# Optimization experiments

Hardware: AMD Instinct MI355X
Metric: run time of the kernel (lower is better)

## Reference

```python
import jax, jax.numpy as jnp
import numpy as np


def setup_inputs() -> dict:
    key = jax.random.key(0)
    ks = jax.random.split(key, 4)
    B, S, H = 1, 2048, 2048
    E, I = 32, 768
    scale_h = 1.0 / np.sqrt(H)
    scale_i = 1.0 / np.sqrt(I)
    return {
        "hidden_states": jax.random.normal(ks[0], (B, S, H), dtype=jnp.float32),
        "gate_w": jax.random.normal(ks[1], (E, H), dtype=jnp.float32) * scale_h,
        "gate_up_proj": jax.random.normal(ks[2], (E, H, 2 * I), dtype=jnp.float32) * scale_h,
        "down_proj": jax.random.normal(ks[3], (E, I, H), dtype=jnp.float32) * scale_i,
    }


TOP_K = 4


def reference(hidden_states, gate_w, gate_up_proj, down_proj):
    B, S, H = hidden_states.shape
    x = hidden_states.reshape(-1, H)                      # [T, H]
    T = x.shape[0]

    # Router: softmax -> top-k -> renormalize -> scatter back to dense [T, E]
    router_logits = x @ gate_w.T                          # [T, E]
    probs = jax.nn.softmax(router_logits.astype(jnp.float32), axis=-1)
    top_w, top_idx = jax.lax.top_k(probs, TOP_K)          # [T, K]
    top_w = top_w / jnp.sum(top_w, axis=-1, keepdims=True)
    top_w = top_w.astype(x.dtype)
    router_weights = jnp.zeros_like(router_logits).at[
        jnp.arange(T)[:, None], top_idx
    ].set(top_w)                                          # [T, E]

    # Experts (eval path): every expert processes every token, then weight & sum.
    gate_up = jnp.einsum("th,ehi->eti", x, gate_up_proj)  # [E, T, 2I]
    gate, up = jnp.split(gate_up, 2, axis=-1)
    h = up * jax.nn.silu(gate)                            # [E, T, I]
    expert_out = jnp.einsum("eti,eih->eth", h, down_proj)  # [E, T, H]
    out = jnp.einsum("eth,te->th", expert_out, router_weights)  # [T, H]

    return out.reshape(B, S, H), router_logits
```

## Files before the change

kernel.cpp:

```cpp
#include <hip/hip_runtime.h>
#include <hip/hip_bf16.h>

#define T_TOK 2048
#define H_DIM 2048
#define E_NUM 32
#define I_DIM 768
#define TOPK  4
#define S4    (T_TOK * TOPK)

typedef __attribute__((ext_vector_type(8))) short bf16x8;
typedef __attribute__((ext_vector_type(4))) float f32x4;

__device__ __forceinline__ unsigned pk2(float a, float b) {
    __hip_bfloat16 ha = __float2bfloat16(a);
    __hip_bfloat16 hb = __float2bfloat16(b);
    unsigned short ua = *(unsigned short*)&ha;
    unsigned short ub = *(unsigned short*)&hb;
    return (unsigned)ua | ((unsigned)ub << 16);
}

__device__ __forceinline__ void gld16(const void* g, void* l) {
    __builtin_amdgcn_global_load_lds(
        (const __attribute__((address_space(1))) void*)g,
        (__attribute__((address_space(3))) void*)l, 16, 0, 0);
}

__global__ __launch_bounds__(256) void zero_kernel(uint4* __restrict__ p, int n16)
{
    int i = blockIdx.x * 256 + threadIdx.x;
    if (i < n16) p[i] = (uint4){0u, 0u, 0u, 0u};
}

__global__ __launch_bounds__(64) void router_kernel(
    const float* __restrict__ x, const float* __restrict__ gate_w,
    float* __restrict__ logits_out, int* __restrict__ cnt,
    int* __restrict__ tok_list, float* __restrict__ tok_w)
{
    const int t = blockIdx.x;
    const int lane = threadIdx.x;
    __shared__ float xs[H_DIM];
    const float4* __restrict__ xv = (const float4*)(x + (size_t)t * H_DIM);
    float4* xsv = (float4*)xs;
#pragma unroll
    for (int i = 0; i < H_DIM / 4 / 64; ++i) xsv[lane + i * 64] = xv[lane + i * 64];
    __syncthreads();

    const int e = lane & 31;
    const int half = lane >> 5;
    const float4* __restrict__ wv = (const float4*)(gate_w + (size_t)e * H_DIM) + half * (H_DIM / 8);
    const float4* __restrict__ xh = ((const float4*)xs) + half * (H_DIM / 8);
    float acc = 0.f;
#pragma unroll 4
    for (int i = 0; i < H_DIM / 8; ++i) {
        float4 w4 = wv[i], x4 = xh[i];
        acc += w4.x * x4.x + w4.y * x4.y + w4.z * x4.z + w4.w * x4.w;
    }
    acc += __shfl_xor(acc, 32, 64);
    if (lane < 32) logits_out[(size_t)t * E_NUM + e] = acc;

    float v = acc;
    float topv[TOPK]; int topi[TOPK];
#pragma unroll
    for (int r = 0; r < TOPK; ++r) {
        float bv = v; int bi = e;
#pragma unroll
        for (int off = 16; off >= 1; off >>= 1) {
            float ov = __shfl_xor(bv, off, 32);
            int   oi = __shfl_xor(bi, off, 32);
            if (ov > bv || (ov == bv && oi < bi)) { bv = ov; bi = oi; }
        }
        topv[r] = bv; topi[r] = bi;
        if (e == bi) v = -1e30f;
    }
    if (lane == 0) {
        float w[TOPK]; float s = 0.f;
#pragma unroll
        for (int r = 0; r < TOPK; ++r) { w[r] = expf(topv[r] - topv[0]); s += w[r]; }
        float inv = 1.f / s;
#pragma unroll
        for (int r = 0; r < TOPK; ++r) {
            int pos = atomicAdd(&cnt[topi[r]], 1);
            tok_list[topi[r] * T_TOK + pos] = t;
            tok_w  [topi[r] * T_TOK + pos] = w[r] * inv;
        }
    }
}

__global__ void scan_kernel(const int* __restrict__ cnt, int* __restrict__ slot_base)
{
    if (threadIdx.x == 0) {
        int s = 0;
        for (int e = 0; e < E_NUM; ++e) { slot_base[e] = s; s += cnt[e]; }
        slot_base[E_NUM] = s;
    }
}

__global__ __launch_bounds__(256) void gather_kernel(
    const float* __restrict__ x, const int* __restrict__ cnt,
    const int* __restrict__ slot_base, const int* __restrict__ tok_list,
    unsigned short* __restrict__ xg_t)
{
    const int e = blockIdx.x;
    const int count = cnt[e];
    const int m0 = blockIdx.y * 8;
    if (m0 >= count) return;
    const int s8   = threadIdx.x >> 5;
    const int kc31 = threadIdx.x & 31;
    const int m = m0 + s8;
    if (m >= count) return;
    const int tok  = tok_list[e * T_TOK + m];
    const int slot = slot_base[e] + m;
    const float* __restrict__ src = x + (size_t)tok * H_DIM;
#pragma unroll
    for (int kcq = 0; kcq < 8; ++kcq) {
        const int kc = kcq * 32 + kc31;
        float4 a = *(const float4*)(src + kc * 8);
        float4 b = *(const float4*)(src + kc * 8 + 4);
        uint4 o;
        o.x = pk2(a.x, a.y); o.y = pk2(a.z, a.w);
        o.z = pk2(b.x, b.y); o.w = pk2(b.z, b.w);
        *(uint4*)(xg_t + ((size_t)kc * S4 + slot) * 8) = o;
    }
}

#define GU_NT (H_DIM / 32)
__global__ __launch_bounds__(512, 6) void gateup_mfma(
    const unsigned short* __restrict__ xg_t, const float* __restrict__ gup_w,
    const int* __restrict__ cnt, const int* __restrict__ slot_base,
    const float* __restrict__ tok_w, unsigned short* __restrict__ h_t)
{
    const int e  = blockIdx.x;
    const int nt = blockIdx.y;
    const int mt = blockIdx.z;
    const int count = cnt[e];
    if (mt * 256 >= count) return;
    const int tid  = threadIdx.x;
    const int lane = tid & 63;
    const int w    = tid >> 6;
    const int base = slot_base[e];
    const int l16  = lane & 15, lg = lane >> 4;

    __shared__ unsigned short As[2][4 * 256 * 8];
    __shared__ unsigned short Bg[2][4 * 32 * 8];
    __shared__ unsigned short Bu[2][4 * 32 * 8];
    __shared__ float wls[256];

    if (tid < 256) {
        int m = mt * 256 + tid; if (m >= count) m = count - 1;
        wls[tid] = tok_w[e * T_TOK + m];
    }

    const int kc = w >> 1;
    const int q0 = (w & 1) * 2;
    int r0 = mt * 256 + q0 * 64 + lane;       if (r0 >= count) r0 = count - 1;
    int r1 = mt * 256 + (q0 + 1) * 64 + lane; if (r1 >= count) r1 = count - 1;
    const unsigned short* ag0 = xg_t + (size_t)kc * (S4 * 8) + (size_t)(base + r0) * 8;
    const unsigned short* ag1 = xg_t + (size_t)kc * (S4 * 8) + (size_t)(base + r1) * 8;
    const int al0 = (kc * 256 + q0 * 64) * 8;
    const int al1 = (kc * 256 + (q0 + 1) * 64) * 8;
    const size_t astep = (size_t)4 * S4 * 8;

    const bool bstage = tid < 256;
    const int bhalf = (tid >> 7) & 1;
    const int t7    = tid & 127;
    const int kb    = (t7 >> 3) * 2;
    const int n4    = (t7 & 7) * 4;
    const int kcb   = kb >> 3;
    const int k8    = kb & 7;
    const float* __restrict__ bsrc =
        gup_w + ((size_t)e * H_DIM + kb) * (2 * I_DIM) + (size_t)bhalf * I_DIM + nt * 32 + n4;

    const int aoff = (lg * 256 + w * 32 + l16) * 8;
    const int boff = (lg * 32 + l16) * 8;

    f32x4 accg[2][2], accu[2][2];
#pragma unroll
    for (int i = 0; i < 2; ++i)
#pragma unroll
        for (int f = 0; f < 2; ++f) { accg[i][f] = {0.f,0.f,0.f,0.f}; accu[i][f] = {0.f,0.f,0.f,0.f}; }

    float4 pr0, pr1;

    gld16(ag0, &As[0][al0]);
    gld16(ag1, &As[0][al1]);
    if (bstage) {
        pr0 = *(const float4*)bsrc;
        pr1 = *(const float4*)(bsrc + 2 * I_DIM);
        unsigned short* bw = bhalf ? &Bu[0][0] : &Bg[0][0];
        float p0[4] = {pr0.x, pr0.y, pr0.z, pr0.w};
        float p1[4] = {pr1.x, pr1.y, pr1.z, pr1.w};
#pragma unroll
        for (int j = 0; j < 4; ++j)
            *(unsigned*)&bw[((kcb * 32 + n4 + j) * 8) + k8] = pk2(p0[j], p1[j]);
    }

    for (int ks = 0; ks < GU_NT; ++ks) {
        const int cur = ks & 1;
        __syncthreads();
        if (ks + 1 < GU_NT) {
            gld16(ag0 + (size_t)(ks + 1) * astep, &As[cur ^ 1][al0]);
            gld16(ag1 + (size_t)(ks + 1) * astep, &As[cur ^ 1][al1]);
            if (bstage) {
                const float* bs_ = bsrc + (size_t)(ks + 1) * 32 * (2 * I_DIM);
                pr0 = *(const float4*)bs_;
                pr1 = *(const float4*)(bs_ + 2 * I_DIM);
            }
        }
        {
            const unsigned short* af_ = &As[cur][aoff];
            const unsigned short* bg_ = &Bg[cur][boff];
            const unsigned short* bu_ = &Bu[cur][boff];
            bf16x8 vg0 = *(const bf16x8*)(bg_);
            bf16x8 vg1 = *(const bf16x8*)(bg_ + 128);
            bf16x8 vu0 = *(const bf16x8*)(bu_);
            bf16x8 vu1 = *(const bf16x8*)(bu_ + 128);
#pragma unroll
            for (int i = 0; i < 2; ++i) {
                bf16x8 va = *(const bf16x8*)(af_ + i * 16 * 8);
                accg[i][0] = __builtin_amdgcn_mfma_f32_16x16x32_bf16(va, vg0, accg[i][0], 0, 0, 0);
                accg[i][1] = __builtin_amdgcn_mfma_f32_16x16x32_bf16(va, vg1, accg[i][1], 0, 0, 0);
                accu[i][0] = __builtin_amdgcn_mfma_f32_16x16x32_bf16(va, vu0, accu[i][0], 0, 0, 0);
                accu[i][1] = __builtin_amdgcn_mfma_f32_16x16x32_bf16(va, vu1, accu[i][1], 0, 0, 0);
            }
        }
        if (ks + 1 < GU_NT && bstage) {
            unsigned short* bw = bhalf ? &Bu[cur ^ 1][0] : &Bg[cur ^ 1][0];
            float p0[4] = {pr0.x, pr0.y, pr0.z, pr0.w};
            float p1[4] = {pr1.x, pr1.y, pr1.z, pr1.w};
#pragma unroll
            for (int j = 0; j < 4; ++j)
                *(unsigned*)&bw[((kcb * 32 + n4 + j) * 8) + k8] = pk2(p0[j], p1[j]);
        }
    }

#pragma unroll
    for (int i = 0; i < 2; ++i) {
        const int mloc = w * 32 + i * 16 + lg * 4;
#pragma unroll
        for (int r = 0; r < 4; ++r) {
            const int mrow = mt * 256 + mloc + r;
            if (mrow < count) {
                const float wgt = wls[mloc + r];
                const size_t slot = (size_t)(base + mrow);
#pragma unroll
                for (int f = 0; f < 2; ++f) {
                    const int col = nt * 32 + f * 16 + l16;
                    float g = accg[i][f][r], u = accu[i][f][r];
                    float sv = g / (1.f + expf(-g));
                    __hip_bfloat16 hb = __float2bfloat16(wgt * u * sv);
                    h_t[((size_t)(col >> 3) * S4 + slot) * 8 + (col & 7)] = *(unsigned short*)&hb;
                }
            }
        }
    }
}

#define DN_NT (I_DIM / 32)
__global__ __launch_bounds__(512, 6) void down_mfma(
    const unsigned short* __restrict__ h_t, const float* __restrict__ down_w,
    const int* __restrict__ cnt, const int* __restrict__ slot_base,
    const int* __restrict__ tok_list, float* __restrict__ out)
{
    const int e  = blockIdx.x;
    const int nt = blockIdx.y;
    const int mt = blockIdx.z;
    const int count = cnt[e];
    if (mt * 256 >= count) return;
    const int tid  = threadIdx.x;
    const int lane = tid & 63;
    const int w    = tid >> 6;
    const int base = slot_base[e];
    const int l16  = lane & 15, lg = lane >> 4;

    __shared__ unsigned short As[2][4 * 256 * 8];
    __shared__ unsigned short Bs[2][4 * 64 * 8];
    __shared__ int toks[256];

    if (tid < 256) {
        int m = mt * 256 + tid; if (m >= count) m = count - 1;
        toks[tid] = tok_list[e * T_TOK + m];
    }

    const int kc = w >> 1;
    const int q0 = (w & 1) * 2;
    int r0 = mt * 256 + q0 * 64 + lane;       if (r0 >= count) r0 = count - 1;
    int r1 = mt * 256 + (q0 + 1) * 64 + lane; if (r1 >= count) r1 = count - 1;
    const unsigned short* ag0 = h_t + (size_t)kc * (S4 * 8) + (size_t)(base + r0) * 8;
    const unsigned short* ag1 = h_t + (size_t)kc * (S4 * 8) + (size_t)(base + r1) * 8;
    const int al0 = (kc * 256 + q0 * 64) * 8;
    const int al1 = (kc * 256 + (q0 + 1) * 64) * 8;
    const size_t astep = (size_t)4 * S4 * 8;

    const bool bstage = tid < 256;
    const int t8  = tid & 255;
    const int kb  = (t8 >> 4) * 2;
    const int n4  = (t8 & 15) * 4;
    const int kcb = kb >> 3;
    const int k8  = kb & 7;
    const float* __restrict__ bsrc =
        down_w + ((size_t)e * I_DIM + kb) * H_DIM + nt * 64 + n4;

    const int aoff = (lg * 256 + w * 32 + l16) * 8;
    const int boff = (lg * 64 + l16) * 8;

    f32x4 acc[2][4];
#pragma unroll
    for (int i = 0; i < 2; ++i)
#pragma unroll
        for (int f = 0; f < 4; ++f) acc[i][f] = {0.f,0.f,0.f,0.f};

    float4 pr0, pr1;

    gld16(ag0, &As[0][al0]);
    gld16(ag1, &As[0][al1]);
    if (bstage) {
        pr0 = *(const float4*)bsrc;
        pr1 = *(const float4*)(bsrc + H_DIM);
        float p0[4] = {pr0.x, pr0.y, pr0.z, pr0.w};
        float p1[4] = {pr1.x, pr1.y, pr1.z, pr1.w};
#pragma unroll
        for (int j = 0; j < 4; ++j)
            *(unsigned*)&Bs[0][((kcb * 64 + n4 + j) * 8) + k8] = pk2(p0[j], p1[j]);
    }

    for (int ks = 0; ks < DN_NT; ++ks) {
        const int cur = ks & 1;
        __syncthreads();
        if (ks + 1 < DN_NT) {
            gld16(ag0 + (size_t)(ks + 1) * astep, &As[cur ^ 1][al0]);
            gld16(ag1 + (size_t)(ks + 1) * astep, &As[cur ^ 1][al1]);
            if (bstage) {
                const float* bs_ = bsrc + (size_t)(ks + 1) * 32 * H_DIM;
                pr0 = *(const float4*)bs_;
                pr1 = *(const float4*)(bs_ + H_DIM);
            }
        }
        {
            const unsigned short* af_ = &As[cur][aoff];
            const unsigned short* bf_ = &Bs[cur][boff];
            bf16x8 vb0 = *(const bf16x8*)(bf_);
            bf16x8 vb1 = *(const bf16x8*)(bf_ + 128);
            bf16x8 vb2 = *(const bf16x8*)(bf_ + 256);
            bf16x8 vb3 = *(const bf16x8*)(bf_ + 384);
#pragma unroll
            for (int i = 0; i < 2; ++i) {
                bf16x8 va = *(const bf16x8*)(af_ + i * 16 * 8);
                acc[i][0] = __builtin_amdgcn_mfma_f32_16x16x32_bf16(va, vb0, acc[i][0], 0, 0, 0);
                acc[i][1] = __builtin_amdgcn_mfma_f32_16x16x32_bf16(va, vb1, acc[i][1], 0, 0, 0);
                acc[i][2] = __builtin_amdgcn_mfma_f32_16x16x32_bf16(va, vb2, acc[i][2], 0, 0, 0);
                acc[i][3] = __builtin_amdgcn_mfma_f32_16x16x32_bf16(va, vb3, acc[i][3], 0, 0, 0);
            }
        }
        if (ks + 1 < DN_NT && bstage) {
            float p0[4] = {pr0.x, pr0.y, pr0.z, pr0.w};
            float p1[4] = {pr1.x, pr1.y, pr1.z, pr1.w};
#pragma unroll
            for (int j = 0; j < 4; ++j)
                *(unsigned*)&Bs[cur ^ 1][((kcb * 64 + n4 + j) * 8) + k8] = pk2(p0[j], p1[j]);
        }
    }

#pragma unroll
    for (int i = 0; i < 2; ++i) {
        const int mloc = w * 32 + i * 16 + lg * 4;
#pragma unroll
        for (int r = 0; r < 4; ++r) {
            const int mrow = mt * 256 + mloc + r;
            if (mrow < count) {
                const int tok = toks[mloc + r];
#pragma unroll
                for (int f = 0; f < 4; ++f) {
                    const int col = nt * 64 + f * 16 + l16;
                    atomicAdd(&out[(size_t)tok * H_DIM + col], acc[i][f][r]);
                }
            }
        }
    }
}

extern "C" void kernel_launch(void* const* d_in, const int* in_sizes, int n_in,
                              void* d_out, int out_size, void* d_ws, size_t ws_size,
                              hipStream_t stream) {
    const float* x      = (const float*)d_in[0];
    const float* gate_w = (const float*)d_in[1];
    const float* gup_w  = (const float*)d_in[2];
    const float* down_w = (const float*)d_in[3];
    float* out    = (float*)d_out;

    char* wsp = (char*)d_ws;
    int*   cnt       = (int*)(wsp);
    int*   slot_base = (int*)(wsp + 256);
    int*   tok_list  = (int*)(wsp + 4096);
    float* tok_w     = (float*)(wsp + 4096 + (size_t)E_NUM * T_TOK * 4);
    unsigned short* xg_t = (unsigned short*)(wsp + (1u << 20));
    unsigned short* h_t  = (unsigned short*)(wsp + (1u << 20) + (size_t)S4 * H_DIM * 2);

    const int n16 = T_TOK * H_DIM / 4;
    zero_kernel<<<(n16 + 255) / 256, 256, 0, stream>>>((uint4*)out, n16);
    hipMemsetAsync(cnt, 0, 256, stream);

    router_kernel<<<T_TOK, 64, 0, stream>>>(x, gate_w, out + (size_t)T_TOK * H_DIM,
                                            cnt, tok_list, tok_w);
    scan_kernel<<<1, 64, 0, stream>>>(cnt, slot_base);
    gather_kernel<<<dim3(E_NUM, 256), 256, 0, stream>>>(x, cnt, slot_base, tok_list, xg_t);
    gateup_mfma<<<dim3(E_NUM, 24, 8), 512, 0, stream>>>(
        xg_t, gup_w, cnt, slot_base, tok_w, h_t);
    down_mfma<<<dim3(E_NUM, 32, 8), 512, 0, stream>>>(
        h_t, down_w, cnt, slot_base, tok_list, out);
}
```

Measured before the change: 518.0 us.

## Loop over token tiles inside each expert block with smaller 128-row tiles

```diff
diff --git a/kernel.cpp b/kernel.cpp
--- a/kernel.cpp
+++ b/kernel.cpp
@@ -124,44 +124,32 @@
 }
 
 #define GU_NT (H_DIM / 32)
-__global__ __launch_bounds__(512, 6) void gateup_mfma(
+__global__ __launch_bounds__(256, 6) void gateup_mfma(
     const unsigned short* __restrict__ xg_t, const float* __restrict__ gup_w,
     const int* __restrict__ cnt, const int* __restrict__ slot_base,
     const float* __restrict__ tok_w, unsigned short* __restrict__ h_t)
 {
     const int e  = blockIdx.x;
     const int nt = blockIdx.y;
-    const int mt = blockIdx.z;
     const int count = cnt[e];
-    if (mt * 256 >= count) return;
+    const int nmt = (count + 127) >> 7;
     const int tid  = threadIdx.x;
     const int lane = tid & 63;
     const int w    = tid >> 6;
     const int base = slot_base[e];
     const int l16  = lane & 15, lg = lane >> 4;
 
-    __shared__ unsigned short As[2][4 * 256 * 8];
+    __shared__ unsigned short As[2][4 * 128 * 8];
     __shared__ unsigned short Bg[2][4 * 32 * 8];
     __shared__ unsigned short Bu[2][4 * 32 * 8];
-    __shared__ float wls[256];
-
-    if (tid < 256) {
-        int m = mt * 256 + tid; if (m >= count) m = count - 1;
-        wls[tid] = tok_w[e * T_TOK + m];
-    }
-
-    const int kc = w >> 1;
-    const int q0 = (w & 1) * 2;
-    int r0 = mt * 256 + q0 * 64 + lane;       if (r0 >= count) r0 = count - 1;
-    int r1 = mt * 256 + (q0 + 1) * 64 + lane; if (r1 >= count) r1 = count - 1;
-    const unsigned short* ag0 = xg_t + (size_t)kc * (S4 * 8) + (size_t)(base + r0) * 8;
-    const unsigned short* ag1 = xg_t + (size_t)kc * (S4 * 8) + (size_t)(base + r1) * 8;
-    const int al0 = (kc * 256 + q0 * 64) * 8;
-    const int al1 = (kc * 256 + (q0 + 1) * 64) * 8;
+    __shared__ float wls[128];
+
+    const unsigned short* agb = xg_t + (size_t)w * (S4 * 8) + (size_t)base * 8;
+    const int al0 = (w * 128 + 0) * 8;
+    const int al1 = (w * 128 + 64) * 8;
     const size_t astep = (size_t)4 * S4 * 8;
 
-    const bool bstage = tid < 256;
-    const int bhalf = (tid >> 7) & 1;
+    const int bhalf = tid >> 7;
     const int t7    = tid & 127;
     const int kb    = (t7 >> 3) * 2;
     const int n4    = (t7 & 7) * 4;
@@ -170,208 +158,215 @@
     const float* __restrict__ bsrc =
         gup_w + ((size_t)e * H_DIM + kb) * (2 * I_DIM) + (size_t)bhalf * I_DIM + nt * 32 + n4;
 
-    const int aoff = (lg * 256 + w * 32 + l16) * 8;
+    const int aoff = (lg * 128 + w * 32 + l16) * 8;
     const int boff = (lg * 32 + l16) * 8;
 
-    f32x4 accg[2][2], accu[2][2];
-#pragma unroll
-    for (int i = 0; i < 2; ++i)
-#pragma unroll
-        for (int f = 0; f < 2; ++f) { accg[i][f] = {0.f,0.f,0.f,0.f}; accu[i][f] = {0.f,0.f,0.f,0.f}; }
-
-    float4 pr0, pr1;
-
-    gld16(ag0, &As[0][al0]);
-    gld16(ag1, &As[0][al1]);
-    if (bstage) {
-        pr0 = *(const float4*)bsrc;
-        pr1 = *(const float4*)(bsrc + 2 * I_DIM);
-        unsigned short* bw = bhalf ? &Bu[0][0] : &Bg[0][0];
-        float p0[4] = {pr0.x, pr0.y, pr0.z, pr0.w};
-        float p1[4] = {pr1.x, pr1.y, pr1.z, pr1.w};
-#pragma unroll
-        for (int j = 0; j < 4; ++j)
-            *(unsigned*)&bw[((kcb * 32 + n4 + j) * 8) + k8] = pk2(p0[j], p1[j]);
-    }
-
-    for (int ks = 0; ks < GU_NT; ++ks) {
-        const int cur = ks & 1;
+    for (int mt = 0; mt < nmt; ++mt) {
         __syncthreads();
-        if (ks + 1 < GU_NT) {
-            gld16(ag0 + (size_t)(ks + 1) * astep, &As[cur ^ 1][al0]);
-            gld16(ag1 + (size_t)(ks + 1) * astep, &As[cur ^ 1][al1]);
-            if (bstage) {
+        if (tid < 128) {
+            int m = mt * 128 + tid; if (m >= count) m = count - 1;
+            wls[tid] = tok_w[e * T_TOK + m];
+        }
+        int r0 = mt * 128 + lane;      if (r0 >= count) r0 = count - 1;
+        int r1 = mt * 128 + 64 + lane; if (r1 >= count) r1 = count - 1;
+        const unsigned short* ag0 = agb + (size_t)r0 * 8;
+        const unsigned short* ag1 = agb + (size_t)r1 * 8;
+
+        f32x4 accg[2][2], accu[2][2];
+#pragma unroll
+        for (int i = 0; i < 2; ++i)
+#pragma unroll
+            for (int f = 0; f < 2; ++f) { accg[i][f] = {0.f,0.f,0.f,0.f}; accu[i][f] = {0.f,0.f,0.f,0.f}; }
+
+        float4 pr0, pr1;
+
+        gld16(ag0, &As[0][al0]);
+        gld16(ag1, &As[0][al1]);
+        {
+            pr0 = *(const float4*)bsrc;
+            pr1 = *(const float4*)(bsrc + 2 * I_DIM);
+            unsigned short* bw = bhalf ? &Bu[0][0] : &Bg[0][0];
+            float p0[4] = {pr0.x, pr0.y, pr0.z, pr0.w};
+            float p1[4] = {pr1.x, pr1.y, pr1.z, pr1.w};
+#pragma unroll
+            for (int j = 0; j < 4; ++j)
+                *(unsigned*)&bw[((kcb * 32 + n4 + j) * 8) + k8] = pk2(p0[j], p1[j]);
+        }
+
+        for (int ks = 0; ks < GU_NT; ++ks) {
+            const int cur = ks & 1;
+            __syncthreads();
+            if (ks + 1 < GU_NT) {
+                gld16(ag0 + (size_t)(ks + 1) * astep, &As[cur ^ 1][al0]);
+                gld16(ag1 + (size_t)(ks + 1) * astep, &As[cur ^ 1][al1]);
                 const float* bs_ = bsrc + (size_t)(ks + 1) * 32 * (2 * I_DIM);
                 pr0 = *(const float4*)bs_;
                 pr1 = *(const float4*)(bs_ + 2 * I_DIM);
             }
-        }
-        {
-            const unsigned short* af_ = &As[cur][aoff];
-            const unsigned short* bg_ = &Bg[cur][boff];
-            const unsigned short* bu_ = &Bu[cur][boff];
-            bf16x8 vg0 = *(const bf16x8*)(bg_);
-            bf16x8 vg1 = *(const bf16x8*)(bg_ + 128);
-            bf16x8 vu0 = *(const bf16x8*)(bu_);
-            bf16x8 vu1 = *(const bf16x8*)(bu_ + 128);
-#pragma unroll
-            for (int i = 0; i < 2; ++i) {
-                bf16x8 va = *(const bf16x8*)(af_ + i * 16 * 8);
-                accg[i][0] = __builtin_amdgcn_mfma_f32_16x16x32_bf16(va, vg0, accg[i][0], 0, 0, 0);
-                accg[i][1] = __builtin_amdgcn_mfma_f32_16x16x32_bf16(va, vg1, accg[i][1], 0, 0, 0);
-                accu[i][0] = __builtin_amdgcn_mfma_f32_16x16x32_bf16(va, vu0, accu[i][0], 0, 0, 0);
-                accu[i][1] = __builtin_amdgcn_mfma_f32_16x16x32_bf16(va, vu1, accu[i][1], 0, 0, 0);
-            }
-        }
-        if (ks + 1 < GU_NT && bstage) {
-            unsigned short* bw = bhalf ? &Bu[cur ^ 1][0] : &Bg[cur ^ 1][0];
-            float p0[4] = {pr0.x, pr0.y, pr0.z, pr0.w};
-            float p1[4] = {pr1.x, pr1.y, pr1.z, pr1.w};
-#pragma unroll
-            for (int j = 0; j < 4; ++j)
-                *(unsigned*)&bw[((kcb * 32 + n4 + j) * 8) + k8] = pk2(p0[j], p1[j]);
-        }
-    }
-
-#pragma unroll
-    for (int i = 0; i < 2; ++i) {
-        const int mloc = w * 32 + i * 16 + lg * 4;
-#pragma unroll
-        for (int r = 0; r < 4; ++r) {
-            const int mrow = mt * 256 + mloc + r;
-            if (mrow < count) {
-                const float wgt = wls[mloc + r];
-                const size_t slot = (size_t)(base + mrow);
-#pragma unroll
-                for (int f = 0; f < 2; ++f) {
-                    const int col = nt * 32 + f * 16 + l16;
-                    float g = accg[i][f][r], u = accu[i][f][r];
-                    float sv = g / (1.f + expf(-g));
-                    __hip_bfloat16 hb = __float2bfloat16(wgt * u * sv);
-                    h_t[((size_t)(col >> 3) * S4 + slot) * 8 + (col & 7)] = *(unsigned short*)&hb;
+            {
+                const unsigned short* af_ = &As[cur][aoff];
+                const unsigned short* bg_ = &Bg[cur][boff];
+                const unsigned short* bu_ = &Bu[cur][boff];
+                bf16x8 vg0 = *(const bf16x8*)(bg_);
+                bf16x8 vg1 = *(const bf16x8*)(bg_ + 128);
+                bf16x8 vu0 = *(const bf16x8*)(bu_);
+                bf16x8 vu1 = *(const bf16x8*)(bu_ + 128);
+#pragma unroll
+                for (int i = 0; i < 2; ++i) {
+                    bf16x8 va = *(const bf16x8*)(af_ + i * 16 * 8);
+                    accg[i][0] = __builtin_amdgcn_mfma_f32_16x16x32_bf16(va, vg0, accg[i][0], 0, 0, 0);
+                    accg[i][1] = __builtin_amdgcn_mfma_f32_16x16x32_bf16(va, vg1, accg[i][1], 0, 0, 0);
+                    accu[i][0] = __builtin_amdgcn_mfma_f32_16x16x32_bf16(va, vu0, accu[i][0], 0, 0, 0);
+                    accu[i][1] = __builtin_amdgcn_mfma_f32_16x16x32_bf16(va, vu1, accu[i][1], 0, 0, 0);
                 }
             }
+            if (ks + 1 < GU_NT) {
+                unsigned short* bw = bhalf ? &Bu[cur ^ 1][0] : &Bg[cur ^ 1][0];
+                float p0[4] = {pr0.x, pr0.y, pr0.z, pr0.w};
+                float p1[4] = {pr1.x, pr1.y, pr1.z, pr1.w};
+#pragma unroll
+                for (int j = 0; j < 4; ++j)
+                    *(unsigned*)&bw[((kcb * 32 + n4 + j) * 8) + k8] = pk2(p0[j], p1[j]);
+            }
+        }
+
+#pragma unroll
+        for (int i = 0; i < 2; ++i) {
+            const int mloc = w * 32 + i * 16 + lg * 4;
+#pragma unroll
+            for (int r = 0; r < 4; ++r) {
+                const int mrow = mt * 128 + mloc + r;
+                if (mrow < count) {
+                    const float wgt = wls[mloc + r];
+                    const size_t slot = (size_t)(base + mrow);
+#pragma unroll
+                    for (int f = 0; f < 2; ++f) {
+                        const int col = nt * 32 + f * 16 + l16;
+                        float g = accg[i][f][r], u = accu[i][f][r];
+                        float sv = g / (1.f + expf(-g));
+                        __hip_bfloat16 hb = __float2bfloat16(wgt * u * sv);
+                        h_t[((size_t)(col >> 3) * S4 + slot) * 8 + (col & 7)] = *(unsigned short*)&hb;
+                    }
+                }
+            }
         }
     }
 }
 
 #define DN_NT (I_DIM / 32)
-__global__ __launch_bounds__(512, 6) void down_mfma(
+__global__ __launch_bounds__(256, 6) void down_mfma(
     const unsigned short* __restrict__ h_t, const float* __restrict__ down_w,
     const int* __restrict__ cnt, const int* __restrict__ slot_base,
     const int* __restrict__ tok_list, float* __restrict__ out)
 {
     const int e  = blockIdx.x;
     const int nt = blockIdx.y;
-    const int mt = blockIdx.z;
     const int count = cnt[e];
-    if (mt * 256 >= count) return;
+    const int nmt = (count + 127) >> 7;
     const int tid  = threadIdx.x;
     const int lane = tid & 63;
     const int w    = tid >> 6;
     const int base = slot_base[e];
     const int l16  = lane & 15, lg = lane >> 4;
 
-    __shared__ unsigned short As[2][4 * 256 * 8];
+    __shared__ unsigned short As[2][4 * 128 * 8];
     __shared__ unsigned short Bs[2][4 * 64 * 8];
-    __shared__ int toks[256];
-
-    if (tid < 256) {
-        int m = mt * 256 + tid; if (m >= count) m = count - 1;
-        toks[tid] = tok_list[e * T_TOK + m];
-    }
-
-    const int kc = w >> 1;
-    const int q0 = (w & 1) * 2;
-    int r0 = mt * 256 + q0 * 64 + lane;       if (r0 >= count) r0 = count - 1;
-    int r1 = mt * 256 + (q0 + 1) * 64 + lane; if (r1 >= count) r1 = count - 1;
-    const unsigned short* ag0 = h_t + (size_t)kc * (S4 * 8) + (size_t)(base + r0) * 8;
-    const unsigned short* ag1 = h_t + (size_t)kc * (S4 * 8) + (size_t)(base + r1) * 8;
-    const int al0 = (kc * 256 + q0 * 64) * 8;
-    const int al1 = (kc * 256 + (q0 + 1) * 64) * 8;
+    __shared__ int toks[128];
+
+    const unsigned short* agb = h_t + (size_t)w * (S4 * 8) + (size_t)base * 8;
+    const int al0 = (w * 128 + 0) * 8;
+    const int al1 = (w * 128 + 64) * 8;
     const size_t astep = (size_t)4 * S4 * 8;
 
-    const bool bstage = tid < 256;
-    const int t8  = tid & 255;
-    const int kb  = (t8 >> 4) * 2;
-    const int n4  = (t8 & 15) * 4;
+    const int kb  = (tid >> 4) * 2;
+    const int n4  = (tid & 15) * 4;
     const int kcb = kb >> 3;
     const int k8  = kb & 7;
     const float* __restrict__ bsrc =
         down_w + ((size_t)e * I_DIM + kb) * H_DIM + nt * 64 + n4;
 
-    const int aoff = (lg * 256 + w * 32 + l16) * 8;
+    const int aoff = (lg * 128 + w * 32 + l16) * 8;
     const int boff = (lg * 64 + l16) * 8;
 
-    f32x4 acc[2][4];
-#pragma unroll
-    for (int i = 0; i < 2; ++i)
-#pragma unroll
-        for (int f = 0; f < 4; ++f) acc[i][f] = {0.f,0.f,0.f,0.f};
-
-    float4 pr0, pr1;
-
-    gld16(ag0, &As[0][al0]);
-    gld16(ag1, &As[0][al1]);
-    if (bstage) {
-        pr0 = *(const float4*)bsrc;
-        pr1 = *(const float4*)(bsrc + H_DIM);
-        float p0[4] = {pr0.x, pr0.y, pr0.z, pr0.w};
-        float p1[4] = {pr1.x, pr1.y, pr1.z, pr1.w};
-#pragma unroll
-        for (int j = 0; j < 4; ++j)
-            *(unsigned*)&Bs[0][((kcb * 64 + n4 + j) * 8) + k8] = pk2(p0[j], p1[j]);
-    }
-
-    for (int ks = 0; ks < DN_NT; ++ks) {
-        const int cur = ks & 1;
+    for (int mt = 0; mt < nmt; ++mt) {
         __syncthreads();
-        if (ks + 1 < DN_NT) {
-            gld16(ag0 + (size_t)(ks + 1) * astep, &As[cur ^ 1][al0]);
-            gld16(ag1 + (size_t)(ks + 1) * astep, &As[cur ^ 1][al1]);
-            if (bstage) {
+        if (tid < 128) {
+            int m = mt * 128 + tid; if (m >= count) m = count - 1;
+            toks[tid] = tok_list[e * T_TOK + m];
+        }
+        int r0 = mt * 128 + lane;      if (r0 >= count) r0 = count - 1;
+        int r1 = mt * 128 + 64 + lane; if (r1 >= count) r1 = count - 1;
+        const unsigned short* ag0 = agb + (size_t)r0 * 8;
+        const unsigned short* ag1 = agb + (size_t)r1 * 8;
+
+        f32x4 acc[2][4];
+#pragma unroll
+        for (int i = 0; i < 2; ++i)
+#pragma unroll
+            for (int f = 0; f < 4; ++f) acc[i][f] = {0.f,0.f,0.f,0.f};
+
+        float4 pr0, pr1;
+
+        gld16(ag0, &As[0][al0]);
+        gld16(ag1, &As[0][al1]);
+        {
+            pr0 = *(const float4*)bsrc;
+            pr1 = *(const float4*)(bsrc + H_DIM);
+            float p0[4] = {pr0.x, pr0.y, pr0.z, pr0.w};
+            float p1[4] = {pr1.x, pr1.y, pr1.z, pr1.w};
+#pragma unroll
+            for (int j = 0; j < 4; ++j)
+                *(unsigned*)&Bs[0][((kcb * 64 + n4 + j) * 8) + k8] = pk2(p0[j], p1[j]);
+        }
+
+        for (int ks = 0; ks < DN_NT; ++ks) {
+            const int cur = ks & 1;
+            __syncthreads();
+            if (ks + 1 < DN_NT) {
+                gld16(ag0 + (size_t)(ks + 1) * astep, &As[cur ^ 1][al0]);
+                gld16(ag1 + (size_t)(ks + 1) * astep, &As[cur ^ 1][al1]);
                 const float* bs_ = bsrc + (size_t)(ks + 1) * 32 * H_DIM;
                 pr0 = *(const float4*)bs_;
                 pr1 = *(const float4*)(bs_ + H_DIM);
             }
-        }
-        {
-            const unsigned short* af_ = &As[cur][aoff];
-            const unsigned short* bf_ = &Bs[cur][boff];
-            bf16x8 vb0 = *(const bf16x8*)(bf_);
-            bf16x8 vb1 = *(const bf16x8*)(bf_ + 128);
-            bf16x8 vb2 = *(const bf16x8*)(bf_ + 256);
-            bf16x8 vb3 = *(const bf16x8*)(bf_ + 384);
-#pragma unroll
-            for (int i = 0; i < 2; ++i) {
-                bf16x8 va = *(const bf16x8*)(af_ + i * 16 * 8);
-                acc[i][0] = __builtin_amdgcn_mfma_f32_16x16x32_bf16(va, vb0, acc[i][0], 0, 0, 0);
-                acc[i][1] = __builtin_amdgcn_mfma_f32_16x16x32_bf16(va, vb1, acc[i][1], 0, 0, 0);
-                acc[i][2] = __builtin_amdgcn_mfma_f32_16x16x32_bf16(va, vb2, acc[i][2], 0, 0, 0);
-                acc[i][3] = __builtin_amdgcn_mfma_f32_16x16x32_bf16(va, vb3, acc[i][3], 0, 0, 0);
-            }
-        }
-        if (ks + 1 < DN_NT && bstage) {
-            float p0[4] = {pr0.x, pr0.y, pr0.z, pr0.w};
-            float p1[4] = {pr1.x, pr1.y, pr1.z, pr1.w};
-#pragma unroll
-            for (int j = 0; j < 4; ++j)
-                *(unsigned*)&Bs[cur ^ 1][((kcb * 64 + n4 + j) * 8) + k8] = pk2(p0[j], p1[j]);
-        }
-    }
-
-#pragma unroll
-    for (int i = 0; i < 2; ++i) {
-        const int mloc = w * 32 + i * 16 + lg * 4;
-#pragma unroll
-        for (int r = 0; r < 4; ++r) {
-            const int mrow = mt * 256 + mloc + r;
-            if (mrow < count) {
-                const int tok = toks[mloc + r];
-#pragma unroll
-                for (int f = 0; f < 4; ++f) {
-                    const int col = nt * 64 + f * 16 + l16;
-                    atomicAdd(&out[(size_t)tok * H_DIM + col], acc[i][f][r]);
+            {
+                const unsigned short* af_ = &As[cur][aoff];
+                const unsigned short* bf_ = &Bs[cur][boff];
+                bf16x8 vb0 = *(const bf16x8*)(bf_);
+                bf16x8 vb1 = *(const bf16x8*)(bf_ + 128);
+                bf16x8 vb2 = *(const bf16x8*)(bf_ + 256);
+                bf16x8 vb3 = *(const bf16x8*)(bf_ + 384);
+#pragma unroll
+                for (int i = 0; i < 2; ++i) {
+                    bf16x8 va = *(const bf16x8*)(af_ + i * 16 * 8);
+                    acc[i][0] = __builtin_amdgcn_mfma_f32_16x16x32_bf16(va, vb0, acc[i][0], 0, 0, 0);
+                    acc[i][1] = __builtin_amdgcn_mfma_f32_16x16x32_bf16(va, vb1, acc[i][1], 0, 0, 0);
+                    acc[i][2] = __builtin_amdgcn_mfma_f32_16x16x32_bf16(va, vb2, acc[i][2], 0, 0, 0);
+                    acc[i][3] = __builtin_amdgcn_mfma_f32_16x16x32_bf16(va, vb3, acc[i][3], 0, 0, 0);
+                }
+            }
+            if (ks + 1 < DN_NT) {
+                float p0[4] = {pr0.x, pr0.y, pr0.z, pr0.w};
+                float p1[4] = {pr1.x, pr1.y, pr1.z, pr1.w};
+#pragma unroll
+                for (int j = 0; j < 4; ++j)
+                    *(unsigned*)&Bs[cur ^ 1][((kcb * 64 + n4 + j) * 8) + k8] = pk2(p0[j], p1[j]);
+            }
+        }
+
+#pragma unroll
+        for (int i = 0; i < 2; ++i) {
+            const int mloc = w * 32 + i * 16 + lg * 4;
+#pragma unroll
+            for (int r = 0; r < 4; ++r) {
+                const int mrow = mt * 128 + mloc + r;
+                if (mrow < count) {
+                    const int tok = toks[mloc + r];
+#pragma unroll
+                    for (int f = 0; f < 4; ++f) {
+                        const int col = nt * 64 + f * 16 + l16;
+                        atomicAdd(&out[(size_t)tok * H_DIM + col], acc[i][f][r]);
+                    }
                 }
             }
         }
@@ -403,8 +398,8 @@
                                             cnt, tok_list, tok_w);
     scan_kernel<<<1, 64, 0, stream>>>(cnt, slot_base);
     gather_kernel<<<dim3(E_NUM, 256), 256, 0, stream>>>(x, cnt, slot_base, tok_list, xg_t);
-    gateup_mfma<<<dim3(E_NUM, 24, 8), 512, 0, stream>>>(
+    gateup_mfma<<<dim3(E_NUM, 24), 256, 0, stream>>>(
         xg_t, gup_w, cnt, slot_base, tok_w, h_t);
-    down_mfma<<<dim3(E_NUM, 32, 8), 512, 0, stream>>>(
+    down_mfma<<<dim3(E_NUM, 32), 256, 0, stream>>>(
         h_t, down_w, cnt, slot_base, tok_list, out);
 }
```

Result: slower. 680.6 us (+31.4%).

## Flatten expert grids with XCD-aware expert swizzle and raise occupancy hints

Applied to the files above, without the earlier changes.

```diff
diff --git a/kernel.cpp b/kernel.cpp
--- a/kernel.cpp
+++ b/kernel.cpp
@@ -23,6 +23,10 @@
     __builtin_amdgcn_global_load_lds(
         (const __attribute__((address_space(1))) void*)g,
         (__attribute__((address_space(3))) void*)l, 16, 0, 0);
+}
+
+__device__ __forceinline__ int eswz(int bid) {
+    return (bid & 7) | (((bid >> 3) & 3) << 3);
 }
 
 __global__ __launch_bounds__(256) void zero_kernel(uint4* __restrict__ p, int n16)
@@ -100,9 +104,10 @@
     const int* __restrict__ slot_base, const int* __restrict__ tok_list,
     unsigned short* __restrict__ xg_t)
 {
-    const int e = blockIdx.x;
+    const int bid = blockIdx.x;
+    const int e = eswz(bid);
     const int count = cnt[e];
-    const int m0 = blockIdx.y * 8;
+    const int m0 = (bid >> 5) * 8;
     if (m0 >= count) return;
     const int s8   = threadIdx.x >> 5;
     const int kc31 = threadIdx.x & 31;
@@ -124,14 +129,16 @@
 }
 
 #define GU_NT (H_DIM / 32)
-__global__ __launch_bounds__(512, 6) void gateup_mfma(
+__global__ __launch_bounds__(512, 8) void gateup_mfma(
     const unsigned short* __restrict__ xg_t, const float* __restrict__ gup_w,
     const int* __restrict__ cnt, const int* __restrict__ slot_base,
     const float* __restrict__ tok_w, unsigned short* __restrict__ h_t)
 {
-    const int e  = blockIdx.x;
-    const int nt = blockIdx.y;
-    const int mt = blockIdx.z;
+    const int bid = blockIdx.x;
+    const int e    = eswz(bid);
+    const int rest = bid >> 5;
+    const int nt   = rest % 24;
+    const int mt   = rest / 24;
     const int count = cnt[e];
     if (mt * 256 >= count) return;
     const int tid  = threadIdx.x;
@@ -143,12 +150,6 @@
     __shared__ unsigned short As[2][4 * 256 * 8];
     __shared__ unsigned short Bg[2][4 * 32 * 8];
     __shared__ unsigned short Bu[2][4 * 32 * 8];
-    __shared__ float wls[256];
-
-    if (tid < 256) {
-        int m = mt * 256 + tid; if (m >= count) m = count - 1;
-        wls[tid] = tok_w[e * T_TOK + m];
-    }
 
     const int kc = w >> 1;
     const int q0 = (w & 1) * 2;
@@ -240,7 +241,7 @@
         for (int r = 0; r < 4; ++r) {
             const int mrow = mt * 256 + mloc + r;
             if (mrow < count) {
-                const float wgt = wls[mloc + r];
+                const float wgt = tok_w[e * T_TOK + mrow];
                 const size_t slot = (size_t)(base + mrow);
 #pragma unroll
                 for (int f = 0; f < 2; ++f) {
@@ -256,14 +257,16 @@
 }
 
 #define DN_NT (I_DIM / 32)
-__global__ __launch_bounds__(512, 6) void down_mfma(
+__global__ __launch_bounds__(512, 8) void down_mfma(
     const unsigned short* __restrict__ h_t, const float* __restrict__ down_w,
     const int* __restrict__ cnt, const int* __restrict__ slot_base,
     const int* __restrict__ tok_list, float* __restrict__ out)
 {
-    const int e  = blockIdx.x;
-    const int nt = blockIdx.y;
-    const int mt = blockIdx.z;
+    const int bid = blockIdx.x;
+    const int e    = eswz(bid);
+    const int rest = bid >> 5;
+    const int nt   = rest & 31;
+    const int mt   = rest >> 5;
     const int count = cnt[e];
     if (mt * 256 >= count) return;
     const int tid  = threadIdx.x;
@@ -274,12 +277,6 @@
 
     __shared__ unsigned short As[2][4 * 256 * 8];
     __shared__ unsigned short Bs[2][4 * 64 * 8];
-    __shared__ int toks[256];
-
-    if (tid < 256) {
-        int m = mt * 256 + tid; if (m >= count) m = count - 1;
-        toks[tid] = tok_list[e * T_TOK + m];
-    }
 
     const int kc = w >> 1;
     const int q0 = (w & 1) * 2;
@@ -367,7 +364,7 @@
         for (int r = 0; r < 4; ++r) {
             const int mrow = mt * 256 + mloc + r;
             if (mrow < count) {
-                const int tok = toks[mloc + r];
+                const int tok = tok_list[e * T_TOK + mrow];
 #pragma unroll
                 for (int f = 0; f < 4; ++f) {
                     const int col = nt * 64 + f * 16 + l16;
@@ -402,9 +399,9 @@
     router_kernel<<<T_TOK, 64, 0, stream>>>(x, gate_w, out + (size_t)T_TOK * H_DIM,
                                             cnt, tok_list, tok_w);
     scan_kernel<<<1, 64, 0, stream>>>(cnt, slot_base);
-    gather_kernel<<<dim3(E_NUM, 256), 256, 0, stream>>>(x, cnt, slot_base, tok_list, xg_t);
-    gateup_mfma<<<dim3(E_NUM, 24, 8), 512, 0, stream>>>(
+    gather_kernel<<<E_NUM * 256, 256, 0, stream>>>(x, cnt, slot_base, tok_list, xg_t);
+    gateup_mfma<<<E_NUM * 24 * 8, 512, 0, stream>>>(
         xg_t, gup_w, cnt, slot_base, tok_w, h_t);
-    down_mfma<<<dim3(E_NUM, 32, 8), 512, 0, stream>>>(
+    down_mfma<<<E_NUM * 32 * 8, 512, 0, stream>>>(
         h_t, down_w, cnt, slot_base, tok_list, out);
 }
```

Result: slower. 812.2 us (+56.8%).

## Load A fragments directly from global and stage B in 128-deep chunks

Applied to the files above, without the earlier changes.

```diff
diff --git a/kernel.cpp b/kernel.cpp
--- a/kernel.cpp
+++ b/kernel.cpp
@@ -19,11 +19,7 @@
     return (unsigned)ua | ((unsigned)ub << 16);
 }
 
-__device__ __forceinline__ void gld16(const void* g, void* l) {
-    __builtin_amdgcn_global_load_lds(
-        (const __attribute__((address_space(1))) void*)g,
-        (__attribute__((address_space(3))) void*)l, 16, 0, 0);
-}
+#define MFMA16(a, b, c) __builtin_amdgcn_mfma_f32_16x16x32_bf16(a, b, c, 0, 0, 0)
 
 __global__ __launch_bounds__(256) void zero_kernel(uint4* __restrict__ p, int n16)
 {
@@ -123,8 +119,8 @@
     }
 }
 
-#define GU_NT (H_DIM / 32)
-__global__ __launch_bounds__(512, 6) void gateup_mfma(
+#define GU_NC (H_DIM / 128)
+__global__ __launch_bounds__(512, 4) void gateup_mfma(
     const unsigned short* __restrict__ xg_t, const float* __restrict__ gup_w,
     const int* __restrict__ cnt, const int* __restrict__ slot_base,
     const float* __restrict__ tok_w, unsigned short* __restrict__ h_t)
@@ -140,9 +136,7 @@
     const int base = slot_base[e];
     const int l16  = lane & 15, lg = lane >> 4;
 
-    __shared__ unsigned short As[2][4 * 256 * 8];
-    __shared__ unsigned short Bg[2][4 * 32 * 8];
-    __shared__ unsigned short Bu[2][4 * 32 * 8];
+    __shared__ unsigned short Bls[2][2][16 * 32 * 8];
     __shared__ float wls[256];
 
     if (tid < 256) {
@@ -150,28 +144,35 @@
         wls[tid] = tok_w[e * T_TOK + m];
     }
 
-    const int kc = w >> 1;
-    const int q0 = (w & 1) * 2;
-    int r0 = mt * 256 + q0 * 64 + lane;       if (r0 >= count) r0 = count - 1;
-    int r1 = mt * 256 + (q0 + 1) * 64 + lane; if (r1 >= count) r1 = count - 1;
-    const unsigned short* ag0 = xg_t + (size_t)kc * (S4 * 8) + (size_t)(base + r0) * 8;
-    const unsigned short* ag1 = xg_t + (size_t)kc * (S4 * 8) + (size_t)(base + r1) * 8;
-    const int al0 = (kc * 256 + q0 * 64) * 8;
-    const int al1 = (kc * 256 + (q0 + 1) * 64) * 8;
-    const size_t astep = (size_t)4 * S4 * 8;
-
-    const bool bstage = tid < 256;
-    const int bhalf = (tid >> 7) & 1;
+    int m0 = mt * 256 + w * 32 + l16;      if (m0 >= count) m0 = count - 1;
+    int m1 = mt * 256 + w * 32 + 16 + l16; if (m1 >= count) m1 = count - 1;
+    const unsigned short* a0b = xg_t + (size_t)(base + m0) * 8;
+    const unsigned short* a1b = xg_t + (size_t)(base + m1) * 8;
+
+    const int bhalf = tid >> 8;
+    const int sub   = (tid >> 7) & 1;
     const int t7    = tid & 127;
     const int kb    = (t7 >> 3) * 2;
     const int n4    = (t7 & 7) * 4;
-    const int kcb   = kb >> 3;
     const int k8    = kb & 7;
-    const float* __restrict__ bsrc =
+    const int kbh   = kb >> 3;
+    const float* __restrict__ bbase =
         gup_w + ((size_t)e * H_DIM + kb) * (2 * I_DIM) + (size_t)bhalf * I_DIM + nt * 32 + n4;
 
-    const int aoff = (lg * 256 + w * 32 + l16) * 8;
-    const int boff = (lg * 32 + l16) * 8;
+    float4 sv0[2], sv1[2];
+
+#define GU_LOAD(C) do { _Pragma("unroll") for (int q2 = 0; q2 < 2; ++q2) { \
+        const int q = sub + q2 * 2; \
+        const float* s_ = bbase + (size_t)((C) * 128 + q * 32) * (2 * I_DIM); \
+        sv0[q2] = *(const float4*)s_; \
+        sv1[q2] = *(const float4*)(s_ + 2 * I_DIM); } } while (0)
+#define GU_WRITE(BUF) do { _Pragma("unroll") for (int q2 = 0; q2 < 2; ++q2) { \
+        const int q = sub + q2 * 2; \
+        unsigned short* bw_ = &Bls[BUF][bhalf][((q * 4 + kbh) * 32) * 8]; \
+        float p0[4] = {sv0[q2].x, sv0[q2].y, sv0[q2].z, sv0[q2].w}; \
+        float p1[4] = {sv1[q2].x, sv1[q2].y, sv1[q2].z, sv1[q2].w}; \
+        _Pragma("unroll") for (int j = 0; j < 4; ++j) \
+            *(unsigned*)&bw_[(n4 + j) * 8 + k8] = pk2(p0[j], p1[j]); } } while (0)
 
     f32x4 accg[2][2], accu[2][2];
 #pragma unroll
@@ -179,59 +180,37 @@
 #pragma unroll
         for (int f = 0; f < 2; ++f) { accg[i][f] = {0.f,0.f,0.f,0.f}; accu[i][f] = {0.f,0.f,0.f,0.f}; }
 
-    float4 pr0, pr1;
-
-    gld16(ag0, &As[0][al0]);
-    gld16(ag1, &As[0][al1]);
-    if (bstage) {
-        pr0 = *(const float4*)bsrc;
-        pr1 = *(const float4*)(bsrc + 2 * I_DIM);
-        unsigned short* bw = bhalf ? &Bu[0][0] : &Bg[0][0];
-        float p0[4] = {pr0.x, pr0.y, pr0.z, pr0.w};
-        float p1[4] = {pr1.x, pr1.y, pr1.z, pr1.w};
-#pragma unroll
-        for (int j = 0; j < 4; ++j)
-            *(unsigned*)&bw[((kcb * 32 + n4 + j) * 8) + k8] = pk2(p0[j], p1[j]);
-    }
-
-    for (int ks = 0; ks < GU_NT; ++ks) {
-        const int cur = ks & 1;
+    GU_LOAD(0);
+    GU_WRITE(0);
+
+    for (int c = 0; c < GU_NC; ++c) {
+        const int buf = c & 1;
         __syncthreads();
-        if (ks + 1 < GU_NT) {
-            gld16(ag0 + (size_t)(ks + 1) * astep, &As[cur ^ 1][al0]);
-            gld16(ag1 + (size_t)(ks + 1) * astep, &As[cur ^ 1][al1]);
-            if (bstage) {
-                const float* bs_ = bsrc + (size_t)(ks + 1) * 32 * (2 * I_DIM);
-                pr0 = *(const float4*)bs_;
-                pr1 = *(const float4*)(bs_ + 2 * I_DIM);
-            }
-        }
-        {
-            const unsigned short* af_ = &As[cur][aoff];
-            const unsigned short* bg_ = &Bg[cur][boff];
-            const unsigned short* bu_ = &Bu[cur][boff];
-            bf16x8 vg0 = *(const bf16x8*)(bg_);
-            bf16x8 vg1 = *(const bf16x8*)(bg_ + 128);
-            bf16x8 vu0 = *(const bf16x8*)(bu_);
-            bf16x8 vu1 = *(const bf16x8*)(bu_ + 128);
-#pragma unroll
-            for (int i = 0; i < 2; ++i) {
-                bf16x8 va = *(const bf16x8*)(af_ + i * 16 * 8);
-                accg[i][0] = __builtin_amdgcn_mfma_f32_16x16x32_bf16(va, vg0, accg[i][0], 0, 0, 0);
-                accg[i][1] = __builtin_amdgcn_mfma_f32_16x16x32_bf16(va, vg1, accg[i][1], 0, 0, 0);
-                accu[i][0] = __builtin_amdgcn_mfma_f32_16x16x32_bf16(va, vu0, accu[i][0], 0, 0, 0);
-                accu[i][1] = __builtin_amdgcn_mfma_f32_16x16x32_bf16(va, vu1, accu[i][1], 0, 0, 0);
-            }
-        }
-        if (ks + 1 < GU_NT && bstage) {
-            unsigned short* bw = bhalf ? &Bu[cur ^ 1][0] : &Bg[cur ^ 1][0];
-            float p0[4] = {pr0.x, pr0.y, pr0.z, pr0.w};
-            float p1[4] = {pr1.x, pr1.y, pr1.z, pr1.w};
-#pragma unroll
-            for (int j = 0; j < 4; ++j)
-                *(unsigned*)&bw[((kcb * 32 + n4 + j) * 8) + k8] = pk2(p0[j], p1[j]);
-        }
-    }
+        if (c + 1 < GU_NC) GU_LOAD(c + 1);
+#pragma unroll
+        for (int s = 0; s < 4; ++s) {
+            const size_t aoff = (size_t)(c * 16 + s * 4 + lg) * (S4 * 8);
+            bf16x8 a0 = *(const bf16x8*)(a0b + aoff);
+            bf16x8 a1 = *(const bf16x8*)(a1b + aoff);
+            const unsigned short* bg_ = &Bls[buf][0][((s * 4 + lg) * 32 + l16) * 8];
+            const unsigned short* bu_ = &Bls[buf][1][((s * 4 + lg) * 32 + l16) * 8];
+            bf16x8 g0 = *(const bf16x8*)(bg_);
+            bf16x8 g1 = *(const bf16x8*)(bg_ + 128);
+            bf16x8 u0 = *(const bf16x8*)(bu_);
+            bf16x8 u1 = *(const bf16x8*)(bu_ + 128);
+            accg[0][0] = MFMA16(a0, g0, accg[0][0]);
+            accg[0][1] = MFMA16(a0, g1, accg[0][1]);
+            accu[0][0] = MFMA16(a0, u0, accu[0][0]);
+            accu[0][1] = MFMA16(a0, u1, accu[0][1]);
+            accg[1][0] = MFMA16(a1, g0, accg[1][0]);
+            accg[1][1] = MFMA16(a1, g1, accg[1][1]);
+            accu[1][0] = MFMA16(a1, u0, accu[1][0]);
+            accu[1][1] = MFMA16(a1, u1, accu[1][1]);
+        }
+        if (c + 1 < GU_NC) GU_WRITE((c + 1) & 1);
+    }
+#undef GU_LOAD
+#undef GU_WRITE
 
 #pragma unroll
     for (int i = 0; i < 2; ++i) {
@@ -255,8 +234,8 @@
     }
 }
 
-#define DN_NT (I_DIM / 32)
-__global__ __launch_bounds__(512, 6) void down_mfma(
+#define DN_NC (I_DIM / 128)
+__global__ __launch_bounds__(512, 4) void down_mfma(
     const unsigned short* __restrict__ h_t, const float* __restrict__ down_w,
     const int* __restrict__ cnt, const int* __restrict__ slot_base,
     const int* __restrict__ tok_list, float* __restrict__ out)
@@ -272,8 +251,7 @@
     const int base = slot_base[e];
     const int l16  = lane & 15, lg = lane >> 4;
 
-    __shared__ unsigned short As[2][4 * 256 * 8];
-    __shared__ unsigned short Bs[2][4 * 64 * 8];
+    __shared__ unsigned short Bls[2][16 * 64 * 8];
     __shared__ int toks[256];
 
     if (tid < 256) {
@@ -281,27 +259,34 @@
         toks[tid] = tok_list[e * T_TOK + m];
     }
 
-    const int kc = w >> 1;
-    const int q0 = (w & 1) * 2;
-    int r0 = mt * 256 + q0 * 64 + lane;       if (r0 >= count) r0 = count - 1;
-    int r1 = mt * 256 + (q0 + 1) * 64 + lane; if (r1 >= count) r1 = count - 1;
-    const unsigned short* ag0 = h_t + (size_t)kc * (S4 * 8) + (size_t)(base + r0) * 8;
-    const unsigned short* ag1 = h_t + (size_t)kc * (S4 * 8) + (size_t)(base + r1) * 8;
-    const int al0 = (kc * 256 + q0 * 64) * 8;
-    const int al1 = (kc * 256 + (q0 + 1) * 64) * 8;
-    const size_t astep = (size_t)4 * S4 * 8;
-
-    const bool bstage = tid < 256;
+    int m0 = mt * 256 + w * 32 + l16;      if (m0 >= count) m0 = count - 1;
+    int m1 = mt * 256 + w * 32 + 16 + l16; if (m1 >= count) m1 = count - 1;
+    const unsigned short* a0b = h_t + (size_t)(base + m0) * 8;
+    const unsigned short* a1b = h_t + (size_t)(base + m1) * 8;
+
+    const int sub = tid >> 8;
     const int t8  = tid & 255;
     const int kb  = (t8 >> 4) * 2;
     const int n4  = (t8 & 15) * 4;
-    const int kcb = kb >> 3;
     const int k8  = kb & 7;
-    const float* __restrict__ bsrc =
+    const int kbh = kb >> 3;
+    const float* __restrict__ bbase =
         down_w + ((size_t)e * I_DIM + kb) * H_DIM + nt * 64 + n4;
 
-    const int aoff = (lg * 256 + w * 32 + l16) * 8;
-    const int boff = (lg * 64 + l16) * 8;
+    float4 sv0[2], sv1[2];
+
+#define DN_LOAD(C) do { _Pragma("unroll") for (int q2 = 0; q2 < 2; ++q2) { \
+        const int q = sub + q2 * 2; \
+        const float* s_ = bbase + (size_t)((C) * 128 + q * 32) * H_DIM; \
+        sv0[q2] = *(const float4*)s_; \
+        sv1[q2] = *(const float4*)(s_ + H_DIM); } } while (0)
+#define DN_WRITE(BUF) do { _Pragma("unroll") for (int q2 = 0; q2 < 2; ++q2) { \
+        const int q = sub + q2 * 2; \
+        unsigned short* bw_ = &Bls[BUF][((q * 4 + kbh) * 64) * 8]; \
+        float p0[4] = {sv0[q2].x, sv0[q2].y, sv0[q2].z, sv0[q2].w}; \
+        float p1[4] = {sv1[q2].x, sv1[q2].y, sv1[q2].z, sv1[q2].w}; \
+        _Pragma("unroll") for (int j = 0; j < 4; ++j) \
+            *(unsigned*)&bw_[(n4 + j) * 8 + k8] = pk2(p0[j], p1[j]); } } while (0)
 
     f32x4 acc[2][4];
 #pragma unroll
@@ -309,56 +294,36 @@
 #pragma unroll
         for (int f = 0; f < 4; ++f) acc[i][f] = {0.f,0.f,0.f,0.f};
 
-    float4 pr0, pr1;
-
-    gld16(ag0, &As[0][al0]);
-    gld16(ag1, &As[0][al1]);
-    if (bstage) {
-        pr0 = *(const float4*)bsrc;
-        pr1 = *(const float4*)(bsrc + H_DIM);
-        float p0[4] = {pr0.x, pr0.y, pr0.z, pr0.w};
-        float p1[4] = {pr1.x, pr1.y, pr1.z, pr1.w};
-#pragma unroll
-        for (int j = 0; j < 4; ++j)
-            *(unsigned*)&Bs[0][((kcb * 64 + n4 + j) * 8) + k8] = pk2(p0[j], p1[j]);
-    }
-
-    for (int ks = 0; ks < DN_NT; ++ks) {
-        const int cur = ks & 1;
+    DN_LOAD(0);
+    DN_WRITE(0);
+
+    for (int c = 0; c < DN_NC; ++c) {
+        const int buf = c & 1;
         __syncthreads();
-        if (ks + 1 < DN_NT) {
-            gld16(ag0 + (size_t)(ks + 1) * astep, &As[cur ^ 1][al0]);
-            gld16(ag1 + (size_t)(ks + 1) * astep, &As[cur ^ 1][al1]);
-            if (bstage) {
-                const float* bs_ = bsrc + (size_t)(ks + 1) * 32 * H_DIM;
-                pr0 = *(const float4*)bs_;
-                pr1 = *(const float4*)(bs_ + H_DIM);
-            }
-        }
-        {
-            const unsigned short* af_ = &As[cur][aoff];
-            const unsigned short* bf_ = &Bs[cur][boff];
-            bf16x8 vb0 = *(const bf16x8*)(bf_);
-            bf16x8 vb1 = *(const bf16x8*)(bf_ + 128);
-            bf16x8 vb2 = *(const bf16x8*)(bf_ + 256);
-            bf16x8 vb3 = *(const bf16x8*)(bf_ + 384);
-#pragma unroll
-            for (int i = 0; i < 2; ++i) {
-                bf16x8 va = *(const bf16x8*)(af_ + i * 16 * 8);
-                acc[i][0] = __builtin_amdgcn_mfma_f32_16x16x32_bf16(va, vb0, acc[i][0], 0, 0, 0);
-                acc[i][1] = __builtin_amdgcn_mfma_f32_16x16x32_bf16(va, vb1, acc[i][1], 0, 0, 0);
-                acc[i][2] = __builtin_amdgcn_mfma_f32_16x16x32_bf16(va, vb2, acc[i][2], 0, 0, 0);
-                acc[i][3] = __builtin_amdgcn_mfma_f32_16x16x32_bf16(va, vb3, acc[i][3], 0, 0, 0);
-            }
-        }
-        if (ks + 1 < DN_NT && bstage) {
-            float p0[4] = {pr0.x, pr0.y, pr0.z, pr0.w};
-            float p1[4] = {pr1.x, pr1.y, pr1.z, pr1.w};
-#pragma unroll
-            for (int j = 0; j < 4; ++j)
-                *(unsigned*)&Bs[cur ^ 1][((kcb * 64 + n4 + j) * 8) + k8] = pk2(p0[j], p1[j]);
-        }
-    }
+        if (c + 1 < DN_NC) DN_LOAD(c + 1);
+#pragma unroll
+        for (int s = 0; s < 4; ++s) {
+            const size_t aoff = (size_t)(c * 16 + s * 4 + lg) * (S4 * 8);
+            bf16x8 a0 = *(const bf16x8*)(a0b + aoff);
+            bf16x8 a1 = *(const bf16x8*)(a1b + aoff);
+            const unsigned short* bf_ = &Bls[buf][((s * 4 + lg) * 64 + l16) * 8];
+            bf16x8 b0 = *(const bf16x8*)(bf_);
+            bf16x8 b1 = *(const bf16x8*)(bf_ + 128);
+            bf16x8 b2 = *(const bf16x8*)(bf_ + 256);
+            bf16x8 b3 = *(const bf16x8*)(bf_ + 384);
+            acc[0][0] = MFMA16(a0, b0, acc[0][0]);
+            acc[0][1] = MFMA16(a0, b1, acc[0][1]);
+            acc[0][2] = MFMA16(a0, b2, acc[0][2]);
+            acc[0][3] = MFMA16(a0, b3, acc[0][3]);
+            acc[1][0] = MFMA16(a1, b0, acc[1][0]);
+            acc[1][1] = MFMA16(a1, b1, acc[1][1]);
+            acc[1][2] = MFMA16(a1, b2, acc[1][2]);
+            acc[1][3] = MFMA16(a1, b3, acc[1][3]);
+        }
+        if (c + 1 < DN_NC) DN_WRITE((c + 1) & 1);
+    }
+#undef DN_LOAD
+#undef DN_WRITE
 
 #pragma unroll
     for (int i = 0; i < 2; ++i) {
```

After: 467.6 us. -9.7%, faster.
